# Kernel optimization log

Measured on AMD Instinct MI355X. Metric: run time of the kernel, lower is better.

The kernel has to match this reference:

```python
import jax, jax.numpy as jnp
import numpy as np

DIM = 1024
HEADS = 16
D_K = DIM // HEADS


def setup_inputs() -> dict:
    key = jax.random.key(0)
    k1, k2, k3, k4 = jax.random.split(key, 4)
    s = 1.0 / np.sqrt(DIM)
    return {
        "x": jax.random.normal(k1, (8, 1024, DIM), dtype=jnp.float32),
        "w_qkv": jax.random.uniform(k2, (DIM, 3 * DIM), dtype=jnp.float32, minval=-s, maxval=s),
        "w_out": jax.random.uniform(k3, (DIM, DIM), dtype=jnp.float32, minval=-s, maxval=s),
        "b_out": jax.random.uniform(k4, (DIM,), dtype=jnp.float32, minval=-s, maxval=s),
    }


def reference(x, w_qkv, w_out, b_out):
    B, N, _ = x.shape
    scale = D_K ** -0.5
    qkv = x @ w_qkv                                   # [B, N, 3*dim]
    q, k, v = jnp.split(qkv, 3, axis=-1)
    # [B, N, dim] -> [B, H, N, d_k]
    def heads(t):
        return t.reshape(B, N, HEADS, D_K).transpose(0, 2, 1, 3)
    q, k, v = heads(q), heads(k), heads(v)
    dots = jnp.einsum("bhnd,bhmd->bhnm", q, k) * scale  # [B, H, N, N]
    attn = jax.nn.softmax(dots, axis=-1)
    out = jnp.einsum("bhnm,bhmd->bhnd", attn, v)        # [B, H, N, d_k]
    out = out.transpose(0, 2, 1, 3).reshape(B, N, HEADS * D_K)
    return out @ w_out + b_out
```

## Files before the change

### kernel.cpp

```cpp
#include <hip/hip_runtime.h>
#include <hip/hip_bf16.h>
#include <math.h>


typedef __attribute__((ext_vector_type(8))) _Float16 f16x8;
typedef __attribute__((ext_vector_type(4))) _Float16 f16x4;
typedef __attribute__((ext_vector_type(4))) float f32x4;
typedef __attribute__((ext_vector_type(16))) float f32x16;
typedef __attribute__((ext_vector_type(4))) unsigned int u32x4;

struct f16x4x2 { f16x4 a, b; };

#define GLOBAL_LOAD_LDS16(g, l) \
  __builtin_amdgcn_global_load_lds((const __attribute__((address_space(1))) void*)(g), \
                                   (__attribute__((address_space(3))) void*)(l), 16, 0, 0)

__global__ __launch_bounds__(256) void cast_f16(
    const float* __restrict__ in, _Float16* __restrict__ hi, int n4) {
  int i = blockIdx.x * blockDim.x + threadIdx.x;
  int stride = gridDim.x * blockDim.x;
  for (; i < n4; i += stride) {
    float4 v = ((const float4*)in)[i];
    f16x4 h;
    h[0] = (_Float16)v.x; h[1] = (_Float16)v.y;
    h[2] = (_Float16)v.z; h[3] = (_Float16)v.w;
    ((f16x4*)hi)[i] = h;
  }
}

__global__ __launch_bounds__(256) void cast_t_f16(
    const float* __restrict__ in, int R, int C, _Float16* __restrict__ hi) {
  __shared__ _Float16 hs[64][65];
  const int r0 = blockIdx.y * 64, c0 = blockIdx.x * 64;
  const int t = threadIdx.x;
#pragma unroll
  for (int it = 0; it < 4; ++it) {
    int r = (t >> 4) + it * 16;
    int cc = (t & 15) * 4;
    float4 v = *(const float4*)(in + (size_t)(r0 + r) * C + c0 + cc);
    hs[r][cc + 0] = (_Float16)v.x;
    hs[r][cc + 1] = (_Float16)v.y;
    hs[r][cc + 2] = (_Float16)v.z;
    hs[r][cc + 3] = (_Float16)v.w;
  }
  __syncthreads();
  const int oc = t >> 2;
  const int rr = (t & 3) * 16;
#pragma unroll
  for (int g = 0; g < 2; ++g) {
    f16x8 a;
#pragma unroll
    for (int j = 0; j < 8; ++j) a[j] = hs[rr + g * 8 + j][oc];
    *(f16x8*)(hi + (size_t)(c0 + oc) * R + r0 + rr + g * 8) = a;
  }
}

__global__ __launch_bounds__(256) void gemm1_qkv(
    const _Float16* __restrict__ Ah, const _Float16* __restrict__ Bh,
    _Float16* __restrict__ qkout, _Float16* __restrict__ vTout) {
  __shared__ char lds[34816];
  const int K = 1024;
  const int tid = threadIdx.x;
  const int wave = tid >> 6, lane = tid & 63;
  const int m0 = blockIdx.y * 128, n0 = blockIdx.x * 128;
  const int wr = wave >> 1, wc = wave & 1;

  const int srow = lane >> 2;
  const int sgchunk = (lane & 3) ^ ((srow >> 1) & 3);
  const int lr = lane & 15, kg = lane >> 4;
  const int rdoff = lr * 64 + ((kg ^ ((lr >> 1) & 3)) * 16);

  f32x4 acc[4][4];
#pragma unroll
  for (int m = 0; m < 4; ++m)
#pragma unroll
    for (int n = 0; n < 4; ++n) acc[m][n] = (f32x4){0.f, 0.f, 0.f, 0.f};

  const _Float16* gbase[2];
  gbase[0] = Ah + (size_t)m0 * K;
  gbase[1] = Bh + (size_t)n0 * K;

  for (int k0 = 0; k0 < K; k0 += 32) {
    __syncthreads();
#pragma unroll
    for (int p = 0; p < 2; ++p) {
#pragma unroll
      for (int half = 0; half < 2; ++half) {
        const int r16 = wave * 32 + half * 16;
        const _Float16* g = gbase[p] + (size_t)(r16 + srow) * K + k0 + sgchunk * 8;
        GLOBAL_LOAD_LDS16(g, lds + p * 8192 + r16 * 64);
      }
    }
    __syncthreads();

    f16x8 af[4], bf[4];
#pragma unroll
    for (int m = 0; m < 4; ++m)
      af[m] = *(const f16x8*)(lds + 0 * 8192 + (wr * 64 + m * 16) * 64 + rdoff);
#pragma unroll
    for (int n = 0; n < 4; ++n)
      bf[n] = *(const f16x8*)(lds + 1 * 8192 + (wc * 64 + n * 16) * 64 + rdoff);
#pragma unroll
    for (int m = 0; m < 4; ++m)
#pragma unroll
      for (int n = 0; n < 4; ++n)
        acc[m][n] = __builtin_amdgcn_mfma_f32_16x16x32_f16(af[m], bf[n], acc[m][n], 0, 0, 0);
  }

  const int crow = (lane >> 4) * 4, ccol = lane & 15;
  if (n0 < 2048) {
#pragma unroll
    for (int m = 0; m < 4; ++m) {
#pragma unroll
      for (int n = 0; n < 4; ++n) {
        const int rbase = m0 + wr * 64 + m * 16 + crow;
        const int c = n0 + wc * 64 + n * 16 + ccol;
#pragma unroll
        for (int i = 0; i < 4; ++i)
          qkout[(size_t)(rbase + i) * 2048 + c] = (_Float16)acc[m][n][i];
      }
    }
  } else {
    __syncthreads();
    _Float16* lv = (_Float16*)lds;
#pragma unroll
    for (int m = 0; m < 4; ++m)
#pragma unroll
      for (int n = 0; n < 4; ++n) {
        const int cc = wc * 64 + n * 16 + ccol;
#pragma unroll
        for (int i = 0; i < 4; ++i) {
          const int r = wr * 64 + m * 16 + crow + i;
          lv[cc * 136 + r] = (_Float16)acc[m][n][i];
        }
      }
    __syncthreads();
    const int bb = m0 >> 10, seq0 = m0 & 1023;
    const int hbase = (n0 - 2048) >> 6;
#pragma unroll
    for (int it = 0; it < 8; ++it) {
      const int idx = tid + it * 256;
      const int cc = idx >> 4, ch = idx & 15;
      f16x8 v = *(const f16x8*)(lv + cc * 136 + ch * 8);
      const int hh = hbase + (cc >> 6), d = cc & 63;
      *(f16x8*)(vTout + (((size_t)bb * 16 + hh) * 64 + d) * 1024 + seq0 + ch * 8) = v;
    }
  }
}

static __device__ inline unsigned pk16(float a, float b) {
  unsigned short ua = __builtin_bit_cast(unsigned short, (_Float16)a);
  unsigned short ub = __builtin_bit_cast(unsigned short, (_Float16)b);
  return (unsigned)ua | ((unsigned)ub << 16);
}

__global__ __launch_bounds__(256) void attn_mfma(
    const _Float16* __restrict__ qk,
    const _Float16* __restrict__ vT,
    _Float16* __restrict__ ao) {
  const int band = blockIdx.x;
  const int h    = blockIdx.y;
  const int b    = blockIdx.z;
  const int tid  = threadIdx.x;
  const int wave = tid >> 6;
  const int lane = tid & 63;
  const int l31  = lane & 31;
  const int hi   = lane >> 5;
  const int kswz = (l31 & 7) << 4;

  __shared__ _Float16 Ks[2][64 * 64];
  __shared__ _Float16 Vt[2][64 * 68];

  const _Float16* vbase = vT + ((size_t)(b * 16 + h) * 64) * 1024;
  const float qscale = 0.125f * 1.44269504088896340736f;

  const int qrow_g = b * 1024 + band * 128 + wave * 32 + l31;
  f16x8 qf[4];
#pragma unroll
  for (int c = 0; c < 4; ++c)
    qf[c] = *(const f16x8*)(qk + (size_t)qrow_g * 2048 + h * 64 + c * 16 + hi * 8);

  f32x16 accO0 = {0}, accO1 = {0};
  float m_run = -INFINITY, l_run = 0.f;

  f16x8 kr[2], vr[2];
  const int sr = tid >> 3, sc8 = tid & 7;

  auto load_t = [&](int t) {
#pragma unroll
    for (int it = 0; it < 2; ++it) {
      const int r = sr + it * 32;
      kr[it] = *(const f16x8*)(qk + (size_t)(b * 1024 + t * 64 + r) * 2048 +
                               1024 + h * 64 + sc8 * 8);
      vr[it] = *(const f16x8*)(vbase + (size_t)r * 1024 + t * 64 + sc8 * 8);
    }
  };
  auto write_buf = [&](int buf) {
#pragma unroll
    for (int it = 0; it < 2; ++it) {
      const int r = sr + it * 32;
      *(f16x8*)((char*)&Ks[buf][0] + r * 128 + ((sc8 * 16) ^ ((r & 7) << 4))) = kr[it];
      f16x4x2 vv = __builtin_bit_cast(f16x4x2, vr[it]);
      char* dst = (char*)&Vt[buf][0] + r * 136 + sc8 * 16;
      *(f16x4*)dst = vv.a;
      *(f16x4*)(dst + 8) = vv.b;
    }
  };

  load_t(0);
  write_buf(0);

  for (int t = 0; t < 16; ++t) {
    if (t < 15) load_t(t + 1);
    __syncthreads();
    const int buf = t & 1;
    const char* ksb = (const char*)&Ks[buf][0];
    const char* vtb = (const char*)&Vt[buf][0];

    f32x16 accS0 = {0}, accS1 = {0};
    __builtin_amdgcn_s_setprio(1);
#pragma unroll
    for (int c = 0; c < 4; ++c) {
      f16x8 ka0 = *(const f16x8*)(ksb + l31 * 128 + ((c * 32 + hi * 16) ^ kswz));
      f16x8 ka1 = *(const f16x8*)(ksb + (l31 + 32) * 128 + ((c * 32 + hi * 16) ^ kswz));
      accS0 = __builtin_amdgcn_mfma_f32_32x32x16_f16(ka0, qf[c], accS0, 0, 0, 0);
      accS1 = __builtin_amdgcn_mfma_f32_32x32x16_f16(ka1, qf[c], accS1, 0, 0, 0);
    }
    __builtin_amdgcn_s_setprio(0);

    float s[32];
#pragma unroll
    for (int r = 0; r < 16; ++r) {
      s[r]      = accS0[r] * qscale;
      s[16 + r] = accS1[r] * qscale;
    }
    float mx4[8];
#pragma unroll
    for (int g = 0; g < 8; ++g)
      mx4[g] = fmaxf(fmaxf(s[4 * g], s[4 * g + 1]), fmaxf(s[4 * g + 2], s[4 * g + 3]));
    float mxa = fmaxf(fmaxf(mx4[0], mx4[1]), fmaxf(mx4[2], mx4[3]));
    float mxb = fmaxf(fmaxf(mx4[4], mx4[5]), fmaxf(mx4[6], mx4[7]));
    float mx = fmaxf(mxa, mxb);
    mx = fmaxf(mx, __shfl_xor(mx, 32));
    const float mn = fmaxf(m_run, mx);
    const float r_resc = __builtin_exp2f(m_run - mn);
    m_run = mn;

    float p[32];
#pragma unroll
    for (int j = 0; j < 32; ++j) p[j] = __builtin_exp2f(s[j] - mn);
    float ps4[8];
#pragma unroll
    for (int g = 0; g < 8; ++g)
      ps4[g] = (p[4 * g] + p[4 * g + 1]) + (p[4 * g + 2] + p[4 * g + 3]);
    float psa = (ps4[0] + ps4[1]) + (ps4[2] + ps4[3]);
    float psb = (ps4[4] + ps4[5]) + (ps4[6] + ps4[7]);
    float ps = psa + psb;
    ps += __shfl_xor(ps, 32);
    l_run = l_run * r_resc + ps;

#pragma unroll
    for (int reg = 0; reg < 16; ++reg) {
      const int qr = (reg & 3) + 8 * (reg >> 2) + 4 * hi;
      const float rb = __shfl(r_resc, qr);
      accO0[reg] *= rb;
      accO1[reg] *= rb;
    }

#pragma unroll
    for (int c = 0; c < 4; ++c) {
      const int j0 = (c >> 1) * 16 + (c & 1) * 8;
      unsigned q0a = pk16(p[j0 + 0], p[j0 + 1]);
      unsigned q0b = pk16(p[j0 + 2], p[j0 + 3]);
      unsigned q1a = pk16(p[j0 + 4], p[j0 + 5]);
      unsigned q1b = pk16(p[j0 + 6], p[j0 + 7]);
      unsigned x0a = __shfl_xor(q0a, 32);
      unsigned x0b = __shfl_xor(q0b, 32);
      unsigned x1a = __shfl_xor(q1a, 32);
      unsigned x1b = __shfl_xor(q1b, 32);
      u32x4 pu;
      if (hi == 0) pu = (u32x4){q0a, q0b, x0a, x0b};
      else         pu = (u32x4){x1a, x1b, q1a, q1b};
      f16x8 pa = __builtin_bit_cast(f16x8, pu);

      const char* vrow0 = vtb + l31 * 136 + (c * 16 + hi * 8) * 2;
      const char* vrow1 = vrow0 + 32 * 136;
      f16x4x2 r0, r1;
      r0.a = *(const f16x4*)vrow0; r0.b = *(const f16x4*)(vrow0 + 8);
      r1.a = *(const f16x4*)vrow1; r1.b = *(const f16x4*)(vrow1 + 8);
      f16x8 vb0 = __builtin_bit_cast(f16x8, r0);
      f16x8 vb1 = __builtin_bit_cast(f16x8, r1);
      __builtin_amdgcn_s_setprio(1);
      accO0 = __builtin_amdgcn_mfma_f32_32x32x16_f16(pa, vb0, accO0, 0, 0, 0);
      accO1 = __builtin_amdgcn_mfma_f32_32x32x16_f16(pa, vb1, accO1, 0, 0, 0);
      __builtin_amdgcn_s_setprio(0);
    }

    if (t < 15) write_buf((t + 1) & 1);
  }

  const float invl = 1.f / l_run;
#pragma unroll
  for (int reg = 0; reg < 16; ++reg) {
    const int qr = (reg & 3) + 8 * (reg >> 2) + 4 * hi;
    const float il = __shfl(invl, qr);
    const size_t grow = (size_t)(b * 1024 + band * 128 + wave * 32 + qr) * 1024 + h * 64;
    ao[grow + l31]      = (_Float16)(accO0[reg] * il);
    ao[grow + 32 + l31] = (_Float16)(accO1[reg] * il);
  }
}

__global__ __launch_bounds__(256) void gemm2_out(
    const _Float16* __restrict__ A,
    const _Float16* __restrict__ B,
    float* __restrict__ C, const float* __restrict__ bias) {
  __shared__ char lds[2 * 8192];
  const int K = 1024;
  const int tid = threadIdx.x;
  const int wave = tid >> 6, lane = tid & 63;
  const int m0 = blockIdx.y * 128, n0 = blockIdx.x * 128;
  const int wr = wave >> 1, wc = wave & 1;

  const int srow = lane >> 2;
  const int sgchunk = (lane & 3) ^ ((srow >> 1) & 3);
  const int lr = lane & 15, kg = lane >> 4;
  const int rdoff = lr * 64 + ((kg ^ ((lr >> 1) & 3)) * 16);

  f32x4 acc[4][4];
#pragma unroll
  for (int m = 0; m < 4; ++m)
#pragma unroll
    for (int n = 0; n < 4; ++n) acc[m][n] = (f32x4){0.f, 0.f, 0.f, 0.f};

  const _Float16* gbase[2];
  gbase[0] = A + (size_t)m0 * K;
  gbase[1] = B + (size_t)n0 * K;

  for (int k0 = 0; k0 < K; k0 += 32) {
    __syncthreads();
#pragma unroll
    for (int p = 0; p < 2; ++p) {
#pragma unroll
      for (int half = 0; half < 2; ++half) {
        const int r16 = wave * 32 + half * 16;
        const _Float16* g = gbase[p] + (size_t)(r16 + srow) * K + k0 + sgchunk * 8;
        GLOBAL_LOAD_LDS16(g, lds + p * 8192 + r16 * 64);
      }
    }
    __syncthreads();

    f16x8 af[4], bf[4];
#pragma unroll
    for (int m = 0; m < 4; ++m)
      af[m] = *(const f16x8*)(lds + 0 * 8192 + (wr * 64 + m * 16) * 64 + rdoff);
#pragma unroll
    for (int n = 0; n < 4; ++n)
      bf[n] = *(const f16x8*)(lds + 1 * 8192 + (wc * 64 + n * 16) * 64 + rdoff);
#pragma unroll
    for (int m = 0; m < 4; ++m)
#pragma unroll
      for (int n = 0; n < 4; ++n)
        acc[m][n] = __builtin_amdgcn_mfma_f32_16x16x32_f16(af[m], bf[n], acc[m][n], 0, 0, 0);
  }

  const int crow = (lane >> 4) * 4, ccol = lane & 15;
#pragma unroll
  for (int m = 0; m < 4; ++m) {
#pragma unroll
    for (int n = 0; n < 4; ++n) {
      const int rbase = m0 + wr * 64 + m * 16 + crow;
      const int c = n0 + wc * 64 + n * 16 + ccol;
      const float bv = bias[c];
#pragma unroll
      for (int i = 0; i < 4; ++i)
        C[(size_t)(rbase + i) * 1024 + c] = acc[m][n][i] + bv;
    }
  }
}

extern "C" void kernel_launch(void* const* d_in, const int* in_sizes, int n_in,
                              void* d_out, int out_size, void* d_ws, size_t ws_size,
                              hipStream_t stream) {
  const float* x     = (const float*)d_in[0];
  const float* w_qkv = (const float*)d_in[1];
  const float* w_out = (const float*)d_in[2];
  const float* b_out = (const float*)d_in[3];
  float* out = (float*)d_out;

  char* ws = (char*)d_ws;
  _Float16* xh  = (_Float16*)(ws);
  _Float16* ao  = xh;
  _Float16* wqT = (_Float16*)(ws + (32u << 20));
  _Float16* woT = (_Float16*)(ws + (44u << 20));
  _Float16* qkp = (_Float16*)(ws + (48u << 20));
  _Float16* vT  = (_Float16*)(ws + (80u << 20));

  cast_f16<<<2048, 256, 0, stream>>>(x, xh, 8192 * 1024 / 4);
  cast_t_f16<<<dim3(48, 16), 256, 0, stream>>>(w_qkv, 1024, 3072, wqT);
  cast_t_f16<<<dim3(16, 16), 256, 0, stream>>>(w_out, 1024, 1024, woT);

  gemm1_qkv<<<dim3(24, 64), 256, 0, stream>>>(xh, wqT, qkp, vT);

  attn_mfma<<<dim3(8, 16, 8), 256, 0, stream>>>(qkp, vT, ao);

  gemm2_out<<<dim3(8, 64), 256, 0, stream>>>(ao, woT, out, b_out);
}
```

Baseline: 207.3 us.

## Fold softmax scale into Q projection, add lazy rescaling and packed conversions

Moves the 1/sqrt(d_k)*log2(e) scale into the QKV GEMM epilogue for Q columns, so the attention kernel no longer multiplies the scores. The online softmax now updates the running max and rescales the output accumulator only when some row's new max exceeds the old one by more than 8 (log2 units), a wave-uniform branch that skips the shuffles and multiplies otherwise. The fp16 packing now uses cvt_pkrtz, and the grid is reordered so blocks for the same band but different head/batch are adjacent. The risks are fp16 overflow headroom from the deferred max (p values can reach 2^8) and round-toward-zero conversion, which changes numerics slightly.

```diff
diff --git a/kernel.cpp b/kernel.cpp
--- a/kernel.cpp
+++ b/kernel.cpp
@@ -10,6 +10,8 @@
 typedef __attribute__((ext_vector_type(4))) unsigned int u32x4;
 
 struct f16x4x2 { f16x4 a, b; };
+
+#define QK_SCALE 0.18033688011112042f
 
 #define GLOBAL_LOAD_LDS16(g, l) \
   __builtin_amdgcn_global_load_lds((const __attribute__((address_space(1))) void*)(g), \
@@ -109,6 +111,7 @@
 
   const int crow = (lane >> 4) * 4, ccol = lane & 15;
   if (n0 < 2048) {
+    const float qsc = (n0 < 1024) ? (float)QK_SCALE : 1.0f;
 #pragma unroll
     for (int m = 0; m < 4; ++m) {
 #pragma unroll
@@ -117,7 +120,7 @@
         const int c = n0 + wc * 64 + n * 16 + ccol;
 #pragma unroll
         for (int i = 0; i < 4; ++i)
-          qkout[(size_t)(rbase + i) * 2048 + c] = (_Float16)acc[m][n][i];
+          qkout[(size_t)(rbase + i) * 2048 + c] = (_Float16)(acc[m][n][i] * qsc);
       }
     }
   } else {
@@ -148,19 +151,14 @@
   }
 }
 
-static __device__ inline unsigned pk16(float a, float b) {
-  unsigned short ua = __builtin_bit_cast(unsigned short, (_Float16)a);
-  unsigned short ub = __builtin_bit_cast(unsigned short, (_Float16)b);
-  return (unsigned)ua | ((unsigned)ub << 16);
-}
-
 __global__ __launch_bounds__(256) void attn_mfma(
     const _Float16* __restrict__ qk,
     const _Float16* __restrict__ vT,
     _Float16* __restrict__ ao) {
-  const int band = blockIdx.x;
-  const int h    = blockIdx.y;
-  const int b    = blockIdx.z;
+  const int hb   = blockIdx.x;
+  const int h    = hb >> 3;
+  const int b    = hb & 7;
+  const int band = blockIdx.y;
   const int tid  = threadIdx.x;
   const int wave = tid >> 6;
   const int lane = tid & 63;
@@ -172,7 +170,6 @@
   __shared__ _Float16 Vt[2][64 * 68];
 
   const _Float16* vbase = vT + ((size_t)(b * 16 + h) * 64) * 1024;
-  const float qscale = 0.125f * 1.44269504088896340736f;
 
   const int qrow_g = b * 1024 + band * 128 + wave * 32 + l31;
   f16x8 qf[4];
@@ -228,52 +225,59 @@
     }
     __builtin_amdgcn_s_setprio(0);
 
-    float s[32];
+    float mx4[8];
+#pragma unroll
+    for (int g = 0; g < 8; ++g) {
+      const float a = (g < 4) ? accS0[4 * g] : accS1[4 * (g - 4)];
+      const float b2 = (g < 4) ? accS0[4 * g + 1] : accS1[4 * (g - 4) + 1];
+      const float c2 = (g < 4) ? accS0[4 * g + 2] : accS1[4 * (g - 4) + 2];
+      const float d2 = (g < 4) ? accS0[4 * g + 3] : accS1[4 * (g - 4) + 3];
+      mx4[g] = fmaxf(fmaxf(a, b2), fmaxf(c2, d2));
+    }
+    float mx = fmaxf(fmaxf(fmaxf(mx4[0], mx4[1]), fmaxf(mx4[2], mx4[3])),
+                     fmaxf(fmaxf(mx4[4], mx4[5]), fmaxf(mx4[6], mx4[7])));
+    mx = fmaxf(mx, __shfl_xor(mx, 32));
+
+    if (!__all(mx - m_run <= 8.f)) {
+      const float mn = fmaxf(m_run, mx);
+      const float r_resc = __builtin_exp2f(m_run - mn);
+      m_run = mn;
+      l_run *= r_resc;
+#pragma unroll
+      for (int reg = 0; reg < 16; ++reg) {
+        const int qr = (reg & 3) + 8 * (reg >> 2) + 4 * hi;
+        const float rb = __shfl(r_resc, qr);
+        accO0[reg] *= rb;
+        accO1[reg] *= rb;
+      }
+    }
+
+    float p[32];
 #pragma unroll
     for (int r = 0; r < 16; ++r) {
-      s[r]      = accS0[r] * qscale;
-      s[16 + r] = accS1[r] * qscale;
-    }
-    float mx4[8];
-#pragma unroll
-    for (int g = 0; g < 8; ++g)
-      mx4[g] = fmaxf(fmaxf(s[4 * g], s[4 * g + 1]), fmaxf(s[4 * g + 2], s[4 * g + 3]));
-    float mxa = fmaxf(fmaxf(mx4[0], mx4[1]), fmaxf(mx4[2], mx4[3]));
-    float mxb = fmaxf(fmaxf(mx4[4], mx4[5]), fmaxf(mx4[6], mx4[7]));
-    float mx = fmaxf(mxa, mxb);
-    mx = fmaxf(mx, __shfl_xor(mx, 32));
-    const float mn = fmaxf(m_run, mx);
-    const float r_resc = __builtin_exp2f(m_run - mn);
-    m_run = mn;
-
-    float p[32];
-#pragma unroll
-    for (int j = 0; j < 32; ++j) p[j] = __builtin_exp2f(s[j] - mn);
+      p[r]      = __builtin_exp2f(accS0[r] - m_run);
+      p[16 + r] = __builtin_exp2f(accS1[r] - m_run);
+    }
     float ps4[8];
 #pragma unroll
     for (int g = 0; g < 8; ++g)
       ps4[g] = (p[4 * g] + p[4 * g + 1]) + (p[4 * g + 2] + p[4 * g + 3]);
-    float psa = (ps4[0] + ps4[1]) + (ps4[2] + ps4[3]);
-    float psb = (ps4[4] + ps4[5]) + (ps4[6] + ps4[7]);
-    float ps = psa + psb;
+    float ps = ((ps4[0] + ps4[1]) + (ps4[2] + ps4[3])) +
+               ((ps4[4] + ps4[5]) + (ps4[6] + ps4[7]));
     ps += __shfl_xor(ps, 32);
-    l_run = l_run * r_resc + ps;
-
-#pragma unroll
-    for (int reg = 0; reg < 16; ++reg) {
-      const int qr = (reg & 3) + 8 * (reg >> 2) + 4 * hi;
-      const float rb = __shfl(r_resc, qr);
-      accO0[reg] *= rb;
-      accO1[reg] *= rb;
-    }
+    l_run += ps;
 
 #pragma unroll
     for (int c = 0; c < 4; ++c) {
       const int j0 = (c >> 1) * 16 + (c & 1) * 8;
-      unsigned q0a = pk16(p[j0 + 0], p[j0 + 1]);
-      unsigned q0b = pk16(p[j0 + 2], p[j0 + 3]);
-      unsigned q1a = pk16(p[j0 + 4], p[j0 + 5]);
-      unsigned q1b = pk16(p[j0 + 6], p[j0 + 7]);
+      unsigned q0a = __builtin_bit_cast(unsigned,
+          __builtin_amdgcn_cvt_pkrtz(p[j0 + 0], p[j0 + 1]));
+      unsigned q0b = __builtin_bit_cast(unsigned,
+          __builtin_amdgcn_cvt_pkrtz(p[j0 + 2], p[j0 + 3]));
+      unsigned q1a = __builtin_bit_cast(unsigned,
+          __builtin_amdgcn_cvt_pkrtz(p[j0 + 4], p[j0 + 5]));
+      unsigned q1b = __builtin_bit_cast(unsigned,
+          __builtin_amdgcn_cvt_pkrtz(p[j0 + 6], p[j0 + 7]));
       unsigned x0a = __shfl_xor(q0a, 32);
       unsigned x0b = __shfl_xor(q0b, 32);
       unsigned x1a = __shfl_xor(q1a, 32);
@@ -401,7 +405,7 @@
 
   gemm1_qkv<<<dim3(24, 64), 256, 0, stream>>>(xh, wqT, qkp, vT);
 
-  attn_mfma<<<dim3(8, 16, 8), 256, 0, stream>>>(qkp, vT, ao);
+  attn_mfma<<<dim3(128, 8), 256, 0, stream>>>(qkp, vT, ao);
 
   gemm2_out<<<dim3(8, 64), 256, 0, stream>>>(ao, woT, out, b_out);
 }
```

Result: faster. 188.5 us (-9.1%).
